# Optimization experiments

Hardware: AMD Instinct MI355X
Metric: run time of the kernel (lower is better)

## Reference

```python
import jax, jax.numpy as jnp
import numpy as np

K = 3; STRIDE = 1; PAD = 1
IN_C = 256; OUT_C = 512
SPAN = K * K * IN_C        # 2304, im2col row count
M = 3                      # ALSH augmentation dims
TABLE_SIZE = 8             # hash buckets
R = 2.5                    # LSH bin width


def setup_inputs() -> dict:
    key = jax.random.key(0)
    k1, k2, k3, k4 = jax.random.split(key, 4)
    stdv = 1.0 / np.sqrt(SPAN)
    inp = jax.random.normal(k1, (16, IN_C, 56, 56), dtype=jnp.float32)
    kernels = jax.random.uniform(k2, (OUT_C, SPAN), minval=-stdv, maxval=stdv,
                                 dtype=jnp.float32)
    a_hash = jax.random.normal(k3, (SPAN + M,), dtype=jnp.float32)
    b_hash = jax.random.uniform(k4, (1,), dtype=jnp.float32) * R
    return {"input": inp, "kernels": kernels, "a_hash": a_hash,
            "b_hash": b_hash, "mode": 1}


def _P(x, m):
    # ALSH P-augmentation: append ||x||^(2^i), i=1..m, per row. x: [O, SPAN]
    n = jnp.linalg.norm(x, axis=1, keepdims=True)
    ext = jnp.concatenate([n ** (2 ** (i + 1)) for i in range(m)], axis=1)
    return jnp.concatenate([x, ext], axis=1)  # [O, SPAN+M]


def _bucket(vals, b, r, ts):
    # floor((v+b)/r) ; fmod ts ; abs  (matches torch fmod-then-abs semantics)
    idx = jnp.floor((vals + b) / r).astype(jnp.int32)
    return jnp.abs(jnp.fmod(idx, ts))


def _im2col_matr(x):
    # [N, C, H, W] -> [SPAN, N*H2*W2]
    n = x.shape[0]
    h2 = (x.shape[2] - K + 2 * PAD) // STRIDE + 1
    w2 = (x.shape[3] - K + 2 * PAD) // STRIDE + 1
    patches = jax.lax.conv_general_dilated_patches(
        x, (K, K), (STRIDE, STRIDE), [(PAD, PAD), (PAD, PAD)])  # [N, SPAN, H2, W2]
    return patches.reshape(n, SPAN, h2 * w2).transpose(1, 0, 2).reshape(SPAN, -1), h2, w2


def reference(input, kernels, a_hash, b_hash, mode):
    n = input.shape[0]
    patch_matr, h2, w2 = _im2col_matr(input)  # [SPAN, L]

    # ---- build ALSH table: bucket of each kernel row ----
    kvals = _P(kernels, M) @ a_hash           # [OUT_C]
    kbuck = _bucket(kvals, b_hash[0], R, TABLE_SIZE)

    # ---- vote: hash every unit-normalized patch column, take modal bucket ----
    unit = patch_matr / jnp.linalg.norm(patch_matr, axis=0, keepdims=True)
    q_ext = jnp.full((M, unit.shape[1]), 0.5, dtype=unit.dtype)
    votes = a_hash @ jnp.concatenate([unit, q_ext], axis=0)  # [L]
    vbuck = _bucket(votes, b_hash[0], R, TABLE_SIZE)
    counts = jnp.bincount(vbuck, length=TABLE_SIZE)
    bucket = int(jnp.argmax(counts))

    # ---- gather active kernel rows for that bucket (data-dependent) ----
    rows = np.sort(np.where(np.asarray(kbuck) == bucket)[0])
    if rows.size != 0:
        active = kernels[jnp.asarray(rows)]          # [oc, SPAN]
        out = active @ patch_matr                    # [oc, L]
        if mode:
            out = out / (float(rows.size) / OUT_C)
        oc = int(rows.size)
    else:
        out = kernels @ patch_matr
        oc = OUT_C

    out = out.reshape(oc, n, h2 * w2).transpose(1, 0, 2).reshape(n, oc, h2, w2)
    return (out, jnp.asarray(rows, dtype=jnp.int32))
```

## Files before the change

kernel.cpp:

```cpp
#include <hip/hip_runtime.h>
#include <math.h>

#define N_    16
#define C_    256
#define H_    56
#define W_    56
#define HW_   3136
#define NPIX  50176
#define OUTC  512
#define SPAN_ 2304
#define BLKPX 256
#define HBYTES 24576
#define PXB   128
#define NPB   (NPIX / PXB)

typedef unsigned short u16;
typedef unsigned int   u32;
typedef __attribute__((ext_vector_type(8))) short bf16x8;
typedef __attribute__((ext_vector_type(8))) unsigned short u16x8;
typedef __attribute__((ext_vector_type(4))) float f32x4;
typedef __attribute__((ext_vector_type(4))) unsigned short u16x4;

__device__ __forceinline__ u16 f2bf(float v) {
    u32 x = __float_as_uint(v);
    u32 r = (x + 0x7fffu + ((x >> 16) & 1u)) >> 16;
    return (u16)r;
}

__device__ __forceinline__ int bucketf(float v, float b) {
    int idx = (int)floorf((v + b) / 2.5f);
    int r = idx % 8;
    return r < 0 ? -r : r;
}

__global__ __launch_bounds__(128) void prep2(const float* __restrict__ x,
                                             const float* __restrict__ ah,
                                             const float* __restrict__ bh,
                                             const float* __restrict__ kern,
                                             u16* __restrict__ xp,
                                             float* __restrict__ g,
                                             float* __restrict__ s2,
                                             int* __restrict__ kbuck,
                                             int* __restrict__ counts) {
    int kb = blockIdx.x - NPB;
    int t = threadIdx.x;
    if (kb >= 0) {
        if (kb == 0 && t < 8) counts[t] = 0;
        int oc_l = t >> 1, part = t & 1;
        int oc = kb * 64 + oc_l;
        const float* kr = kern + (size_t)oc * SPAN_ + part * 1152;
        const float* ap = ah + part * 1152;
        float dot = 0.f, ss = 0.f;
        for (int i = 0; i < 288; ++i) {
            float4 kv = *(const float4*)(kr + i * 4);
            float4 av = *(const float4*)(ap + i * 4);
            dot += kv.x * av.x + kv.y * av.y + kv.z * av.z + kv.w * av.w;
            ss  += kv.x * kv.x + kv.y * kv.y + kv.z * kv.z + kv.w * kv.w;
        }
        dot += __shfl_xor(dot, 1);
        ss  += __shfl_xor(ss, 1);
        if (part == 0) {
            float n2 = ss;
            float n4 = n2 * n2;
            float n8 = n4 * n4;
            float v = dot + n2 * ah[SPAN_] + n4 * ah[SPAN_ + 1] +
                      n8 * ah[SPAN_ + 2];
            kbuck[oc] = bucketf(v, bh[0]);
        }
        return;
    }

    __shared__ float aL[SPAN_];
    __shared__ u16 tl[PXB][68];
    for (int j = t; j < SPAN_; j += 128) aL[j] = ah[j];

    const int px = blockIdx.x * PXB + t;
    const int img = px / HW_;
    const size_t xbase = (size_t)img * C_ * HW_ + (px - img * HW_);

    float pg[9];
#pragma unroll
    for (int kk = 0; kk < 9; ++kk) pg[kk] = 0.f;
    float ps = 0.f;
    __syncthreads();

    for (int ph = 0; ph < 4; ++ph) {
        float R[16], Rn[16];
#pragma unroll
        for (int i = 0; i < 16; ++i)
            R[i] = x[xbase + (size_t)(ph * 64 + i) * HW_];
#pragma unroll
        for (int sub = 0; sub < 4; ++sub) {
            if (sub < 3) {
#pragma unroll
                for (int i = 0; i < 16; ++i)
                    Rn[i] = x[xbase + (size_t)(ph * 64 + (sub + 1) * 16 + i) * HW_];
            }
#pragma unroll
            for (int i = 0; i < 16; ++i) {
                int c = ph * 64 + sub * 16 + i;
                float v = R[i];
                const float* ac = &aL[c * 9];
#pragma unroll
                for (int kk = 0; kk < 9; ++kk) pg[kk] += ac[kk] * v;
                ps += v * v;
                tl[t][sub * 16 + i] = f2bf(v);
            }
            if (sub < 3) {
#pragma unroll
                for (int i = 0; i < 16; ++i) R[i] = Rn[i];
            }
        }
        __syncthreads();
        const int oct = t & 7;
#pragma unroll
        for (int pass = 0; pass < 8; ++pass) {
            int pxl = pass * 16 + (t >> 3);
            u16x8 v8 = *(const u16x8*)&tl[pxl][oct * 8];
            *(u16x8*)&xp[((size_t)(blockIdx.x * PXB + pxl)) * C_ +
                         ph * 64 + oct * 8] = v8;
        }
        __syncthreads();
    }

#pragma unroll
    for (int kk = 0; kk < 9; ++kk) g[(size_t)kk * NPIX + px] = pg[kk];
    s2[px] = ps;
}

__global__ __launch_bounds__(256) void vote_kernel(const float* __restrict__ g,
                                                   const float* __restrict__ s2,
                                                   const float* __restrict__ ah,
                                                   const float* __restrict__ bh,
                                                   int* __restrict__ counts) {
    __shared__ int hist[8];
    if (threadIdx.x < 8) hist[threadIdx.x] = 0;
    __syncthreads();
    int q = blockIdx.x * 256 + threadIdx.x;
    int n = q / HW_;
    int p = q - n * HW_;
    int h = p / W_;
    int w = p - h * W_;
    float dot = 0.f, ss = 0.f;
#pragma unroll
    for (int kk = 0; kk < 9; ++kk) {
        int dh = kk / 3 - 1, dw = kk % 3 - 1;
        int hh = h + dh, ww = w + dw;
        if (hh >= 0 && hh < H_ && ww >= 0 && ww < W_) {
            int idx = n * HW_ + hh * W_ + ww;
            dot += g[(size_t)kk * NPIX + idx];
            ss  += s2[idx];
        }
    }
    float qext = 0.5f * (ah[SPAN_] + ah[SPAN_ + 1] + ah[SPAN_ + 2]);
    float v = dot / sqrtf(ss) + qext;
    int b = bucketf(v, bh[0]);
    atomicAdd(&hist[b], 1);
    __syncthreads();
    if (threadIdx.x < 8) atomicAdd(&counts[threadIdx.x], hist[threadIdx.x]);
}

__global__ __launch_bounds__(256) void prep_w(const float* __restrict__ kern,
                                              const int* __restrict__ kbuck,
                                              const int* __restrict__ counts,
                                              const int* __restrict__ mode,
                                              float* __restrict__ out,
                                              u16* __restrict__ wfrag,
                                              int nfB, int oc_total) {
    __shared__ int sc[256];
    __shared__ int rowsL[512];
    int t = threadIdx.x;
    int best = 0, bc = counts[0];
#pragma unroll
    for (int i = 1; i < 8; ++i) {
        int c = counts[i];
        if (c > bc) { bc = c; best = i; }
    }
    int f0 = (kbuck[t] == best) ? 1 : 0;
    int f1 = (kbuck[t + 256] == best) ? 1 : 0;
    sc[t] = f0 | (f1 << 16);
    __syncthreads();
    for (int off = 1; off < 256; off <<= 1) {
        int add = (t >= off) ? sc[t - off] : 0;
        __syncthreads();
        sc[t] += add;
        __syncthreads();
    }
    int tot = sc[255];
    int t0  = tot & 0xffff;
    int cnt = t0 + (tot >> 16);
    int pos0 = (sc[t] & 0xffff) - f0;
    int pos1 = t0 + (sc[t] >> 16) - f1;
    rowsL[t] = 0; rowsL[t + 256] = 0;
    __syncthreads();
    if (cnt == 0) { rowsL[t] = t; rowsL[t + 256] = t + 256; }
    else {
        if (f0) rowsL[pos0] = t;
        if (f1) rowsL[pos1] = t + 256;
    }
    __syncthreads();
    int ocEff = (cnt == 0) ? OUTC : cnt;
    float scale = (mode[0] && cnt > 0) ? 512.0f / (float)cnt : 1.0f;

    if (blockIdx.x == 0) {
        float* rout = out + (size_t)N_ * oc_total * HW_;
        int nw = ocEff < oc_total ? ocEff : oc_total;
        if (cnt == 0) {
            if (t < nw) rout[t] = (float)t;
            if (t + 256 < nw) rout[t + 256] = (float)(t + 256);
        } else {
            if (f0 && pos0 < nw) rout[pos0] = (float)t;
            if (f1 && pos1 < nw) rout[pos1] = (float)(t + 256);
        }
    }

    int e = blockIdx.x * 256 + t;
    int lane = e & 63;
    int t2 = e >> 6;
    int g = t2 % nfB;
    int s = t2 / nfB;
    int kk = s >> 3;
    int cb = s & 7;
    int q = lane >> 4;
    int mcol = lane & 15;
    int oc_i = g * 16 + mcol;
    bool valid = oc_i < ocEff;
    int row = valid ? rowsL[oc_i] : 0;
    const float* kr = kern + (size_t)row * SPAN_;
    u16 w8[8];
#pragma unroll
    for (int j = 0; j < 8; ++j) {
        int c = cb * 32 + q * 8 + j;
        float v = valid ? kr[c * 9 + kk] * scale : 0.f;
        w8[j] = f2bf(v);
    }
    u16* dst = wfrag + ((size_t)((s * nfB + g) * 64 + lane)) * 8;
#pragma unroll
    for (int j = 0; j < 8; ++j) dst[j] = w8[j];
}

__global__ __launch_bounds__(256, 2) void conv_mfma(const u16* __restrict__ xp,
                                                    const u16* __restrict__ wfrag,
                                                    float* __restrict__ out,
                                                    int nfB, int oc_total, int nby) {
    __shared__ char halo[2 * HBYTES];

    int flat = blockIdx.x;
    int bx, by;
    int full = 192 * nby;
    if (flat < full) {
        int gsz = 8 * nby;
        int gi = flat / gsz;
        int tr = flat - gi * gsz;
        by = tr >> 3;
        bx = gi * 8 + (tr & 7);
    } else {
        int tr = flat - full;
        by = tr >> 2;
        bx = 192 + (tr & 3);
    }

    const int t = threadIdx.x;
    const int lane = t & 63;
    const int wv = t >> 6;
    const int pb = bx * BLKPX;
    const int fb = by * 3;
    const int lane15 = lane & 15;
    const int laneq  = lane >> 4;

    u32 valMask[4];
    int aB[4][3];
#pragma unroll
    for (int f = 0; f < 4; ++f) {
        int p = pb + wv * 64 + f * 16 + lane15;
        int img = p / HW_;
        int rp = p - img * HW_;
        int h = rp / W_;
        int w = rp - h * W_;
        u32 m = 0;
#pragma unroll
        for (int kk = 0; kk < 9; ++kk) {
            int dh = kk / 3 - 1, dw = kk % 3 - 1;
            int hh = h + dh, ww = w + dw;
            if (hh >= 0 && hh < H_ && ww >= 0 && ww < W_) m |= (1u << kk);
        }
        valMask[f] = m;
#pragma unroll
        for (int j = 0; j < 3; ++j) {
            int sn = 57 + wv * 64 + f * 16 + lane15 + (j - 1);
            aB[f][j] = sn * 64 + ((laneq ^ ((sn >> 1) & 3)) << 4) - 3584;
        }
    }

    f32x4 acc[4][3];
#pragma unroll
    for (int f = 0; f < 4; ++f)
#pragma unroll
        for (int gg = 0; gg < 3; ++gg) acc[f][gg] = (f32x4){0.f, 0.f, 0.f, 0.f};
    const bf16x8 zf = {0, 0, 0, 0, 0, 0, 0, 0};

    const char* xpb = (const char*)xp;
    const int q4 = (((t & 3) ^ ((t >> 3) & 3)) << 4);
    int gpx[6];
#pragma unroll
    for (int r = 0; r < 6; ++r) {
        int p = pb - 57 + r * 64 + (t >> 2);
        gpx[r] = p < 0 ? 0 : (p >= NPIX ? NPIX - 1 : p);
    }

#pragma unroll
    for (int r = 0; r < 6; ++r)
        __builtin_amdgcn_global_load_lds(
            (const __attribute__((address_space(1))) unsigned int*)
                (xpb + (size_t)gpx[r] * 512 + q4),
            (__attribute__((address_space(3))) unsigned int*)&halo[r * 4096 + t * 16],
            16, 0, 0);

    const size_t cbStride = (size_t)nfB * 512;
    const size_t kkStride = cbStride * 8;
    const u16* wl = wfrag + (size_t)fb * 512 + (size_t)lane * 8;
    bf16x8 bW[3], bWn[3];
#define LOADB(dst, cb_, kk_) do {                                               \
    const u16* _wp = wl + (size_t)(kk_) * kkStride + (size_t)(cb_) * cbStride;  \
    _Pragma("unroll")                                                           \
    for (int _g = 0; _g < 3; ++_g)                                              \
        dst[_g] = *(const bf16x8*)(_wp + (size_t)_g * 512);                     \
} while (0)

    LOADB(bW, 0, 0);

#pragma unroll
    for (int cb = 0; cb < 8; ++cb) {
        __syncthreads();

        if (cb < 7) {
            const int nb = ((cb + 1) & 1) * HBYTES;
#pragma unroll
            for (int r = 0; r < 6; ++r)
                __builtin_amdgcn_global_load_lds(
                    (const __attribute__((address_space(1))) unsigned int*)
                        (xpb + (size_t)gpx[r] * 512 + (cb + 1) * 64 + q4),
                    (__attribute__((address_space(3))) unsigned int*)
                        &halo[nb + r * 4096 + t * 16],
                    16, 0, 0);
        }

#pragma unroll
        for (int kk = 0; kk < 9; ++kk) {
            if (kk < 8)       LOADB(bWn, cb, kk + 1);
            else if (cb < 7)  LOADB(bWn, cb + 1, 0);

            const int dh = kk / 3 - 1;
            const int j  = kk % 3;
            const int IMM = (cb & 1) * HBYTES + (dh + 1) * 3584;
            bf16x8 aX[4];
#pragma unroll
            for (int f = 0; f < 4; ++f) {
                bf16x8 a = *(const bf16x8*)&halo[aB[f][j] + IMM];
                aX[f] = ((valMask[f] >> kk) & 1) ? a : zf;
            }
#pragma unroll
            for (int gg = 0; gg < 3; ++gg)
#pragma unroll
                for (int f = 0; f < 4; ++f)
                    acc[f][gg] = __builtin_amdgcn_mfma_f32_16x16x32_bf16(
                        aX[f], bW[gg], acc[f][gg], 0, 0, 0);
            if (kk < 8 || cb < 7) {
#pragma unroll
                for (int gg = 0; gg < 3; ++gg) bW[gg] = bWn[gg];
            }
        }
    }
#undef LOADB

#pragma unroll
    for (int f = 0; f < 4; ++f) {
        int p0 = pb + wv * 64 + f * 16 + laneq * 4;
        int img0 = p0 / HW_;
        int hw0 = p0 - img0 * HW_;
#pragma unroll
        for (int gg = 0; gg < 3; ++gg) {
            int oc = (fb + gg) * 16 + lane15;
            if (oc < oc_total) {
                float* op = out + ((size_t)img0 * oc_total + oc) * HW_ + hw0;
                *(f32x4*)op = acc[f][gg];
            }
        }
    }
}

extern "C" void kernel_launch(void* const* d_in, const int* in_sizes, int n_in,
                              void* d_out, int out_size, void* d_ws, size_t ws_size,
                              hipStream_t stream) {
    const float* x    = (const float*)d_in[0];
    const float* kern = (const float*)d_in[1];
    const float* ah   = (const float*)d_in[2];
    const float* bh   = (const float*)d_in[3];
    const int*   mode = (const int*)d_in[4];
    float* out = (float*)d_out;

    int oc_total = (out_size % (N_ * HW_ + 1) == 0) ? out_size / (N_ * HW_ + 1)
                                                    : OUTC;
    int nfTot = (oc_total + 15) / 16;
    int nby   = (nfTot + 2) / 3;
    int nfB   = nby * 3;

    u16*   xp     = (u16*)d_ws;
    u16*   wfrag  = xp + (size_t)NPIX * C_;
    float* g      = (float*)(wfrag + (size_t)72 * 36 * 64 * 8);
    float* s2     = g + (size_t)9 * NPIX;
    int*   counts = (int*)(s2 + NPIX);
    int*   kbuck  = counts + 8;

    prep2<<<NPB + 8, 128, 0, stream>>>(x, ah, bh, kern, xp, g, s2, kbuck,
                                       counts);
    vote_kernel<<<NPIX / 256, 256, 0, stream>>>(g, s2, ah, bh, counts);
    prep_w<<<18 * nfB, 256, 0, stream>>>(kern, kbuck, counts, mode, out, wfrag,
                                         nfB, oc_total);
    conv_mfma<<<(NPIX / BLKPX) * nby, 256, 0, stream>>>(xp, wfrag, out, nfB,
                                                        oc_total, nby);
}
```

Before: 93.47 us.

## Split prep channels across thread groups and use zero-slot halo addressing in conv

The prep kernel now uses 512 threads per block, with four groups each handling 64 channels of the same 128 pixels. Each thread writes its bf16 transposed pixels directly instead of staging through shared memory, and the partial hash dot products are reduced through shared memory. In the conv kernel, out-of-bounds taps are redirected to a zeroed LDS slot, removing the per-tap mask select. Weight fragments are triple-buffered two taps ahead instead of being copied between registers. The precomputed 36-entry address array raises register pressure, and the direct global stores in prep may coalesce less well.

```diff
diff --git a/kernel.cpp b/kernel.cpp
--- a/kernel.cpp
+++ b/kernel.cpp
@@ -11,15 +11,15 @@
 #define SPAN_ 2304
 #define BLKPX 256
 #define HBYTES 24576
-#define PXB   128
-#define NPB   (NPIX / PXB)
+#define ZSLOT 24512
+#define PXB3  128
+#define NPB3  (NPIX / PXB3)
 
 typedef unsigned short u16;
 typedef unsigned int   u32;
 typedef __attribute__((ext_vector_type(8))) short bf16x8;
 typedef __attribute__((ext_vector_type(8))) unsigned short u16x8;
 typedef __attribute__((ext_vector_type(4))) float f32x4;
-typedef __attribute__((ext_vector_type(4))) unsigned short u16x4;
 
 __device__ __forceinline__ u16 f2bf(float v) {
     u32 x = __float_as_uint(v);
@@ -33,7 +33,7 @@
     return r < 0 ? -r : r;
 }
 
-__global__ __launch_bounds__(128) void prep2(const float* __restrict__ x,
+__global__ __launch_bounds__(512) void prep3(const float* __restrict__ x,
                                              const float* __restrict__ ah,
                                              const float* __restrict__ bh,
                                              const float* __restrict__ kern,
@@ -42,23 +42,23 @@
                                              float* __restrict__ s2,
                                              int* __restrict__ kbuck,
                                              int* __restrict__ counts) {
-    int kb = blockIdx.x - NPB;
+    int kb = blockIdx.x - NPB3;
     int t = threadIdx.x;
     if (kb >= 0) {
         if (kb == 0 && t < 8) counts[t] = 0;
-        int oc_l = t >> 1, part = t & 1;
-        int oc = kb * 64 + oc_l;
-        const float* kr = kern + (size_t)oc * SPAN_ + part * 1152;
-        const float* ap = ah + part * 1152;
+        int oc_l = t >> 2, part = t & 3;
+        int oc = kb * 128 + oc_l;
+        const float* kr = kern + (size_t)oc * SPAN_ + part * 576;
+        const float* ap = ah + part * 576;
         float dot = 0.f, ss = 0.f;
-        for (int i = 0; i < 288; ++i) {
+        for (int i = 0; i < 144; ++i) {
             float4 kv = *(const float4*)(kr + i * 4);
             float4 av = *(const float4*)(ap + i * 4);
             dot += kv.x * av.x + kv.y * av.y + kv.z * av.z + kv.w * av.w;
             ss  += kv.x * kv.x + kv.y * kv.y + kv.z * kv.z + kv.w * kv.w;
         }
-        dot += __shfl_xor(dot, 1);
-        ss  += __shfl_xor(ss, 1);
+        dot += __shfl_xor(dot, 1); dot += __shfl_xor(dot, 2);
+        ss  += __shfl_xor(ss, 1);  ss  += __shfl_xor(ss, 2);
         if (part == 0) {
             float n2 = ss;
             float n4 = n2 * n2;
@@ -71,12 +71,15 @@
     }
 
     __shared__ float aL[SPAN_];
-    __shared__ u16 tl[PXB][68];
-    for (int j = t; j < SPAN_; j += 128) aL[j] = ah[j];
-
-    const int px = blockIdx.x * PXB + t;
-    const int img = px / HW_;
+    __shared__ float red[3][PXB3][10];
+    for (int j = t; j < SPAN_; j += 512) aL[j] = ah[j];
+
+    const int px_l = t & 127;
+    const int grp  = t >> 7;
+    const int px   = blockIdx.x * PXB3 + px_l;
+    const int img  = px / HW_;
     const size_t xbase = (size_t)img * C_ * HW_ + (px - img * HW_);
+    const int c0 = grp * 64;
 
     float pg[9];
 #pragma unroll
@@ -84,48 +87,41 @@
     float ps = 0.f;
     __syncthreads();
 
-    for (int ph = 0; ph < 4; ++ph) {
-        float R[16], Rn[16];
+#pragma unroll
+    for (int bt = 0; bt < 4; ++bt) {
+        float R[16];
 #pragma unroll
         for (int i = 0; i < 16; ++i)
-            R[i] = x[xbase + (size_t)(ph * 64 + i) * HW_];
-#pragma unroll
-        for (int sub = 0; sub < 4; ++sub) {
-            if (sub < 3) {
-#pragma unroll
-                for (int i = 0; i < 16; ++i)
-                    Rn[i] = x[xbase + (size_t)(ph * 64 + (sub + 1) * 16 + i) * HW_];
-            }
-#pragma unroll
-            for (int i = 0; i < 16; ++i) {
-                int c = ph * 64 + sub * 16 + i;
-                float v = R[i];
-                const float* ac = &aL[c * 9];
-#pragma unroll
-                for (int kk = 0; kk < 9; ++kk) pg[kk] += ac[kk] * v;
-                ps += v * v;
-                tl[t][sub * 16 + i] = f2bf(v);
-            }
-            if (sub < 3) {
-#pragma unroll
-                for (int i = 0; i < 16; ++i) R[i] = Rn[i];
-            }
-        }
-        __syncthreads();
-        const int oct = t & 7;
-#pragma unroll
-        for (int pass = 0; pass < 8; ++pass) {
-            int pxl = pass * 16 + (t >> 3);
-            u16x8 v8 = *(const u16x8*)&tl[pxl][oct * 8];
-            *(u16x8*)&xp[((size_t)(blockIdx.x * PXB + pxl)) * C_ +
-                         ph * 64 + oct * 8] = v8;
-        }
-        __syncthreads();
-    }
-
-#pragma unroll
-    for (int kk = 0; kk < 9; ++kk) g[(size_t)kk * NPIX + px] = pg[kk];
-    s2[px] = ps;
+            R[i] = x[xbase + (size_t)(c0 + bt * 16 + i) * HW_];
+        u16x8 pa, pb;
+#pragma unroll
+        for (int i = 0; i < 16; ++i) {
+            float v = R[i];
+            const float* ac = &aL[(c0 + bt * 16 + i) * 9];
+#pragma unroll
+            for (int kk = 0; kk < 9; ++kk) pg[kk] += ac[kk] * v;
+            ps += v * v;
+            if (i < 8) pa[i] = f2bf(v); else pb[i - 8] = f2bf(v);
+        }
+        *(u16x8*)&xp[(size_t)px * C_ + c0 + bt * 16]     = pa;
+        *(u16x8*)&xp[(size_t)px * C_ + c0 + bt * 16 + 8] = pb;
+    }
+
+    if (grp > 0) {
+#pragma unroll
+        for (int kk = 0; kk < 9; ++kk) red[grp - 1][px_l][kk] = pg[kk];
+        red[grp - 1][px_l][9] = ps;
+    }
+    __syncthreads();
+    if (grp == 0) {
+#pragma unroll
+        for (int kk = 0; kk < 9; ++kk) {
+            float s = pg[kk] + red[0][px_l][kk] + red[1][px_l][kk] +
+                      red[2][px_l][kk];
+            g[(size_t)kk * NPIX + px] = s;
+        }
+        s2[px] = ps + red[0][px_l][9] + red[1][px_l][9] + red[2][px_l][9];
+    }
 }
 
 __global__ __launch_bounds__(256) void vote_kernel(const float* __restrict__ g,
@@ -268,8 +264,12 @@
     const int lane15 = lane & 15;
     const int laneq  = lane >> 4;
 
-    u32 valMask[4];
-    int aB[4][3];
+    if (t < 8) {
+        int off = ((t & 4) ? HBYTES : 0) + ZSLOT + (t & 3) * 16;
+        *(u16x8*)&halo[off] = (u16x8){0, 0, 0, 0, 0, 0, 0, 0};
+    }
+
+    int addrA[4][9];
 #pragma unroll
     for (int f = 0; f < 4; ++f) {
         int p = pb + wv * 64 + f * 16 + lane15;
@@ -277,18 +277,14 @@
         int rp = p - img * HW_;
         int h = rp / W_;
         int w = rp - h * W_;
-        u32 m = 0;
 #pragma unroll
         for (int kk = 0; kk < 9; ++kk) {
             int dh = kk / 3 - 1, dw = kk % 3 - 1;
             int hh = h + dh, ww = w + dw;
-            if (hh >= 0 && hh < H_ && ww >= 0 && ww < W_) m |= (1u << kk);
-        }
-        valMask[f] = m;
-#pragma unroll
-        for (int j = 0; j < 3; ++j) {
-            int sn = 57 + wv * 64 + f * 16 + lane15 + (j - 1);
-            aB[f][j] = sn * 64 + ((laneq ^ ((sn >> 1) & 3)) << 4) - 3584;
+            bool val = (hh >= 0) & (hh < H_) & (ww >= 0) & (ww < W_);
+            int sn = 57 + wv * 64 + f * 16 + lane15 + dw;
+            int base = sn * 64 + ((laneq ^ ((sn >> 1) & 3)) << 4) - 3584;
+            addrA[f][kk] = val ? base : (ZSLOT - (kk / 3) * 3584);
         }
     }
 
@@ -297,7 +293,6 @@
     for (int f = 0; f < 4; ++f)
 #pragma unroll
         for (int gg = 0; gg < 3; ++gg) acc[f][gg] = (f32x4){0.f, 0.f, 0.f, 0.f};
-    const bf16x8 zf = {0, 0, 0, 0, 0, 0, 0, 0};
 
     const char* xpb = (const char*)xp;
     const int q4 = (((t & 3) ^ ((t >> 3) & 3)) << 4);
@@ -309,25 +304,29 @@
     }
 
 #pragma unroll
-    for (int r = 0; r < 6; ++r)
-        __builtin_amdgcn_global_load_lds(
-            (const __attribute__((address_space(1))) unsigned int*)
-                (xpb + (size_t)gpx[r] * 512 + q4),
-            (__attribute__((address_space(3))) unsigned int*)&halo[r * 4096 + t * 16],
-            16, 0, 0);
+    for (int r = 0; r < 6; ++r) {
+        if (r < 5 || t < 252)
+            __builtin_amdgcn_global_load_lds(
+                (const __attribute__((address_space(1))) unsigned int*)
+                    (xpb + (size_t)gpx[r] * 512 + q4),
+                (__attribute__((address_space(3))) unsigned int*)
+                    &halo[r * 4096 + t * 16],
+                16, 0, 0);
+    }
 
     const size_t cbStride = (size_t)nfB * 512;
     const size_t kkStride = cbStride * 8;
     const u16* wl = wfrag + (size_t)fb * 512 + (size_t)lane * 8;
-    bf16x8 bW[3], bWn[3];
-#define LOADB(dst, cb_, kk_) do {                                               \
+    bf16x8 bB[3][3];
+#define LOADB(slot, cb_, kk_) do {                                              \
     const u16* _wp = wl + (size_t)(kk_) * kkStride + (size_t)(cb_) * cbStride;  \
     _Pragma("unroll")                                                           \
     for (int _g = 0; _g < 3; ++_g)                                              \
-        dst[_g] = *(const bf16x8*)(_wp + (size_t)_g * 512);                     \
+        bB[slot][_g] = *(const bf16x8*)(_wp + (size_t)_g * 512);                \
 } while (0)
 
-    LOADB(bW, 0, 0);
+    LOADB(0, 0, 0);
+    LOADB(1, 0, 1);
 
 #pragma unroll
     for (int cb = 0; cb < 8; ++cb) {
@@ -336,39 +335,33 @@
         if (cb < 7) {
             const int nb = ((cb + 1) & 1) * HBYTES;
 #pragma unroll
-            for (int r = 0; r < 6; ++r)
-                __builtin_amdgcn_global_load_lds(
-                    (const __attribute__((address_space(1))) unsigned int*)
-                        (xpb + (size_t)gpx[r] * 512 + (cb + 1) * 64 + q4),
-                    (__attribute__((address_space(3))) unsigned int*)
-                        &halo[nb + r * 4096 + t * 16],
-                    16, 0, 0);
+            for (int r = 0; r < 6; ++r) {
+                if (r < 5 || t < 252)
+                    __builtin_amdgcn_global_load_lds(
+                        (const __attribute__((address_space(1))) unsigned int*)
+                            (xpb + (size_t)gpx[r] * 512 + (cb + 1) * 64 + q4),
+                        (__attribute__((address_space(3))) unsigned int*)
+                            &halo[nb + r * 4096 + t * 16],
+                        16, 0, 0);
+            }
         }
 
 #pragma unroll
         for (int kk = 0; kk < 9; ++kk) {
-            if (kk < 8)       LOADB(bWn, cb, kk + 1);
-            else if (cb < 7)  LOADB(bWn, cb + 1, 0);
-
-            const int dh = kk / 3 - 1;
-            const int j  = kk % 3;
-            const int IMM = (cb & 1) * HBYTES + (dh + 1) * 3584;
+            if (kk < 7)       LOADB((kk + 2) % 3, cb, kk + 2);
+            else if (cb < 7)  LOADB((kk + 2) % 3, cb + 1, kk - 7);
+
+            const int IMM = (cb & 1) * HBYTES + (kk / 3) * 3584;
             bf16x8 aX[4];
 #pragma unroll
-            for (int f = 0; f < 4; ++f) {
-                bf16x8 a = *(const bf16x8*)&halo[aB[f][j] + IMM];
-                aX[f] = ((valMask[f] >> kk) & 1) ? a : zf;
-            }
+            for (int f = 0; f < 4; ++f)
+                aX[f] = *(const bf16x8*)&halo[addrA[f][kk] + IMM];
 #pragma unroll
             for (int gg = 0; gg < 3; ++gg)
 #pragma unroll
                 for (int f = 0; f < 4; ++f)
                     acc[f][gg] = __builtin_amdgcn_mfma_f32_16x16x32_bf16(
-                        aX[f], bW[gg], acc[f][gg], 0, 0, 0);
-            if (kk < 8 || cb < 7) {
-#pragma unroll
-                for (int gg = 0; gg < 3; ++gg) bW[gg] = bWn[gg];
-            }
+                        aX[f], bB[kk % 3][gg], acc[f][gg], 0, 0, 0);
         }
     }
 #undef LOADB
@@ -412,8 +405,8 @@
     int*   counts = (int*)(s2 + NPIX);
     int*   kbuck  = counts + 8;
 
-    prep2<<<NPB + 8, 128, 0, stream>>>(x, ah, bh, kern, xp, g, s2, kbuck,
-                                       counts);
+    prep3<<<NPB3 + 4, 512, 0, stream>>>(x, ah, bh, kern, xp, g, s2, kbuck,
+                                        counts);
     vote_kernel<<<NPIX / 256, 256, 0, stream>>>(g, s2, ah, bh, counts);
     prep_w<<<18 * nfB, 256, 0, stream>>>(kern, kbuck, counts, mode, out, wfrag,
                                          nfB, oc_total);
```

After: 154.9 us. 1.66x slower.
